# Performance work log

Hardware: AMD Instinct MI355X
Metric: run time of the kernel (lower is better)

The kernel has to match this reference:

```python
import jax, jax.numpy as jnp
import numpy as np

B, N = 2048, 4095  # batch, number of spherical points (cumsum length = N+1)


def setup_inputs() -> dict:
    key = jax.random.key(0)
    k1, k2, k3, k4, k5 = jax.random.split(key, 5)
    return {
        "origin_3D": jax.random.uniform(k1, (B, 3, 1), dtype=jnp.float32),
        "spherical_3D": jax.random.uniform(k2, (B, 3, N), dtype=jnp.float32),
        "origin_2D": jax.random.uniform(k3, (B, 3, 1), dtype=jnp.float32),
        "spherical_2D": jax.random.uniform(k4, (B, 3, N), dtype=jnp.float32),
        "deformation_field": jax.random.uniform(k5, (B, 2, N), dtype=jnp.float32),
    }


def _cart(origin, spherical):
    # spherical: [B, 3, N] with rows (r, theta, phi)
    r, theta, phi = spherical[:, 0, :], spherical[:, 1, :], spherical[:, 2, :]
    st = jnp.sin(theta)
    x = r * st * jnp.cos(phi)
    y = r * st * jnp.sin(phi)
    z = r * jnp.cos(theta)
    shape = jnp.stack((x, y, z), axis=1)            # [B, 3, N]
    full = jnp.concatenate((origin, shape), axis=2)  # [B, 3, N+1]
    # torch.matmul(full, triu(ones)) == prefix sum along the last axis
    return jnp.cumsum(full, axis=2)


def reference(origin_3D, spherical_3D, origin_2D, spherical_2D, deformation_field):
    spherical_3D_deformed = spherical_3D.at[:, 1:, :].add(deformation_field)
    original_cart = _cart(origin_2D, spherical_2D)            # [B, 3, N+1]
    deformed_cart = _cart(origin_3D, spherical_3D_deformed)   # [B, 3, N+1]
    per_pt = jnp.sum(jnp.abs(deformed_cart - original_cart), axis=1)  # [B, N+1]
    return jnp.sum(jnp.mean(per_pt, axis=1))  # scalar
```

## Files before the change

### kernel.cpp

```cpp
#include <hip/hip_runtime.h>


#define BATCH 2048
#define NPTS  4095
#define POS   4096
#define T     512
#define NW    8
#define M     8

__launch_bounds__(T, 2)
__global__ void mpd_loss_kernel(const float* __restrict__ origin3,
                                const float* __restrict__ sph3,
                                const float* __restrict__ origin2,
                                const float* __restrict__ sph2,
                                const float* __restrict__ def,
                                float* __restrict__ bsum) {
    __shared__ float ldsT[3][M][NW];
    __shared__ float wsum[NW];

    const int b    = blockIdx.x;
    const int t    = threadIdx.x;
    const int lane = t & 63;
    const int w    = t >> 6;

    const float* r3  = sph3 + (size_t)b * 3 * NPTS;
    const float* th3 = r3 + NPTS;
    const float* ph3 = th3 + NPTS;
    const float* r2  = sph2 + (size_t)b * 3 * NPTS;
    const float* th2 = r2 + NPTS;
    const float* ph2 = th2 + NPTS;
    const float* d0  = def + (size_t)b * 2 * NPTS;
    const float* d1  = d0 + NPTS;

    float vx[M], vy[M], vz[M];

    #pragma unroll
    for (int m = 0; m < M; ++m) {
        const int j = m * T + t;
        float dx, dy, dz;
        if (m == 0 && t == 0) {
            const float* o3 = origin3 + (size_t)b * 3;
            const float* o2 = origin2 + (size_t)b * 3;
            dx = o3[0] - o2[0];
            dy = o3[1] - o2[1];
            dz = o3[2] - o2[2];
        } else {
            const int n = j - 1;
            const float R3  = r3[n];
            const float Th3 = th3[n] + d0[n];
            const float Ph3 = ph3[n] + d1[n];
            const float R2  = r2[n];
            const float Th2 = th2[n];
            const float Ph2 = ph2[n];
            float s3, c3, sp3, cp3, s2, c2, sp2, cp2;
            __sincosf(Th3, &s3, &c3);
            __sincosf(Ph3, &sp3, &cp3);
            __sincosf(Th2, &s2, &c2);
            __sincosf(Ph2, &sp2, &cp2);
            const float rs3 = R3 * s3;
            const float rs2 = R2 * s2;
            dx = rs3 * cp3 - rs2 * cp2;
            dy = rs3 * sp3 - rs2 * sp2;
            dz = R3 * c3 - R2 * c2;
        }
        vx[m] = dx; vy[m] = dy; vz[m] = dz;
    }

    #pragma unroll
    for (int m = 0; m < M; ++m) {
        float x = vx[m], y = vy[m], z = vz[m];
        #pragma unroll
        for (int off = 1; off < 64; off <<= 1) {
            const float ux = __shfl_up(x, off, 64);
            const float uy = __shfl_up(y, off, 64);
            const float uz = __shfl_up(z, off, 64);
            if (lane >= off) { x += ux; y += uy; z += uz; }
        }
        vx[m] = x; vy[m] = y; vz[m] = z;
        if (lane == 63) {
            ldsT[0][m][w] = x;
            ldsT[1][m][w] = y;
            ldsT[2][m][w] = z;
        }
    }
    __syncthreads();

    float acc = 0.f;
    float rbx = 0.f, rby = 0.f, rbz = 0.f;
    #pragma unroll
    for (int m = 0; m < M; ++m) {
        float wx = 0.f, wy = 0.f, wz = 0.f;
        float tx = 0.f, ty = 0.f, tz = 0.f;
        #pragma unroll
        for (int ww = 0; ww < NW; ++ww) {
            const float a = ldsT[0][m][ww];
            const float c = ldsT[1][m][ww];
            const float e = ldsT[2][m][ww];
            if (ww < w) { wx += a; wy += c; wz += e; }
            tx += a; ty += c; tz += e;
        }
        acc += fabsf(rbx + wx + vx[m]) + fabsf(rby + wy + vy[m]) + fabsf(rbz + wz + vz[m]);
        rbx += tx; rby += ty; rbz += tz;
    }

    #pragma unroll
    for (int off = 32; off > 0; off >>= 1) acc += __shfl_down(acc, off, 64);
    if (lane == 0) wsum[w] = acc;
    __syncthreads();
    if (t == 0) {
        float s = 0.f;
        #pragma unroll
        for (int i = 0; i < NW; ++i) s += wsum[i];
        bsum[b] = s * (1.0f / POS);
    }
}

__launch_bounds__(256)
__global__ void reduce_kernel(const float* __restrict__ bsum, float* __restrict__ out) {
    const int t = threadIdx.x;
    float acc = 0.f;
    #pragma unroll
    for (int i = 0; i < BATCH / 256; ++i) acc += bsum[t + i * 256];
    #pragma unroll
    for (int off = 32; off > 0; off >>= 1) acc += __shfl_down(acc, off, 64);
    __shared__ float wsum[4];
    if ((t & 63) == 0) wsum[t >> 6] = acc;
    __syncthreads();
    if (t == 0) out[0] = wsum[0] + wsum[1] + wsum[2] + wsum[3];
}

extern "C" void kernel_launch(void* const* d_in, const int* in_sizes, int n_in,
                              void* d_out, int out_size, void* d_ws, size_t ws_size,
                              hipStream_t stream) {
    const float* origin3 = (const float*)d_in[0];
    const float* sph3    = (const float*)d_in[1];
    const float* origin2 = (const float*)d_in[2];
    const float* sph2    = (const float*)d_in[3];
    const float* def     = (const float*)d_in[4];
    float* out  = (float*)d_out;
    float* bsum = (float*)d_ws;

    mpd_loss_kernel<<<BATCH, T, 0, stream>>>(origin3, sph3, origin2, sph2, def, bsum);
    reduce_kernel<<<1, 256, 0, stream>>>(bsum, out);
}
```

Baseline: 272.0 us.

## Restructure prefix sum as per-thread serial chunks through padded LDS transpose

Each thread still computes its Cartesian deltas with coalesced global loads, but now writes them to padded LDS buffers. It then reads back a contiguous chunk of 8 elements, sums them serially, and runs only one wave-level shuffle scan on the chunk totals instead of eight. Each element's prefix is then rebuilt by serial accumulation. This cuts shuffle and scan instruction count roughly eightfold. In exchange it adds about 52KB of LDS per block and an extra barrier, and the occupancy hint is raised to 6 blocks, which the LDS footprint may not allow.

```diff
diff --git a/kernel.cpp b/kernel.cpp
--- a/kernel.cpp
+++ b/kernel.cpp
@@ -7,15 +7,20 @@
 #define T     512
 #define NW    8
 #define M     8
+#define CH    8
+#define BUFSZ 4352
 
-__launch_bounds__(T, 2)
+__launch_bounds__(T, 6)
 __global__ void mpd_loss_kernel(const float* __restrict__ origin3,
                                 const float* __restrict__ sph3,
                                 const float* __restrict__ origin2,
                                 const float* __restrict__ sph2,
                                 const float* __restrict__ def,
                                 float* __restrict__ bsum) {
-    __shared__ float ldsT[3][M][NW];
+    __shared__ float bufx[BUFSZ];
+    __shared__ float bufy[BUFSZ];
+    __shared__ float bufz[BUFSZ];
+    __shared__ float wtotx[NW], wtoty[NW], wtotz[NW];
     __shared__ float wsum[NW];
 
     const int b    = blockIdx.x;
@@ -31,8 +36,6 @@
     const float* ph2 = th2 + NPTS;
     const float* d0  = def + (size_t)b * 2 * NPTS;
     const float* d1  = d0 + NPTS;
-
-    float vx[M], vy[M], vz[M];
 
     #pragma unroll
     for (int m = 0; m < M; ++m) {
@@ -63,44 +66,49 @@
             dy = rs3 * sp3 - rs2 * sp2;
             dz = R3 * c3 - R2 * c2;
         }
-        vx[m] = dx; vy[m] = dy; vz[m] = dz;
-    }
-
-    #pragma unroll
-    for (int m = 0; m < M; ++m) {
-        float x = vx[m], y = vy[m], z = vz[m];
-        #pragma unroll
-        for (int off = 1; off < 64; off <<= 1) {
-            const float ux = __shfl_up(x, off, 64);
-            const float uy = __shfl_up(y, off, 64);
-            const float uz = __shfl_up(z, off, 64);
-            if (lane >= off) { x += ux; y += uy; z += uz; }
-        }
-        vx[m] = x; vy[m] = y; vz[m] = z;
-        if (lane == 63) {
-            ldsT[0][m][w] = x;
-            ldsT[1][m][w] = y;
-            ldsT[2][m][w] = z;
-        }
+        const int a = j + (j >> 4);
+        bufx[a] = dx;
+        bufy[a] = dy;
+        bufz[a] = dz;
     }
     __syncthreads();
 
+    const int jb = t * CH;
+    const int ba = jb + (jb >> 4);
+    float vx[CH], vy[CH], vz[CH];
+    float tx = 0.f, ty = 0.f, tz = 0.f;
+    #pragma unroll
+    for (int k = 0; k < CH; ++k) {
+        vx[k] = bufx[ba + k]; tx += vx[k];
+        vy[k] = bufy[ba + k]; ty += vy[k];
+        vz[k] = bufz[ba + k]; tz += vz[k];
+    }
+
+    float ix = tx, iy = ty, iz = tz;
+    #pragma unroll
+    for (int off = 1; off < 64; off <<= 1) {
+        const float ux = __shfl_up(ix, off, 64);
+        const float uy = __shfl_up(iy, off, 64);
+        const float uz = __shfl_up(iz, off, 64);
+        if (lane >= off) { ix += ux; iy += uy; iz += uz; }
+    }
+    if (lane == 63) { wtotx[w] = ix; wtoty[w] = iy; wtotz[w] = iz; }
+    __syncthreads();
+
+    float wox = 0.f, woy = 0.f, woz = 0.f;
+    #pragma unroll
+    for (int ww = 0; ww < NW; ++ww) {
+        if (ww < w) { wox += wtotx[ww]; woy += wtoty[ww]; woz += wtotz[ww]; }
+    }
+
+    float px = wox + (ix - tx);
+    float py = woy + (iy - ty);
+    float pz = woz + (iz - tz);
     float acc = 0.f;
-    float rbx = 0.f, rby = 0.f, rbz = 0.f;
     #pragma unroll
-    for (int m = 0; m < M; ++m) {
-        float wx = 0.f, wy = 0.f, wz = 0.f;
-        float tx = 0.f, ty = 0.f, tz = 0.f;
-        #pragma unroll
-        for (int ww = 0; ww < NW; ++ww) {
-            const float a = ldsT[0][m][ww];
-            const float c = ldsT[1][m][ww];
-            const float e = ldsT[2][m][ww];
-            if (ww < w) { wx += a; wy += c; wz += e; }
-            tx += a; ty += c; tz += e;
-        }
-        acc += fabsf(rbx + wx + vx[m]) + fabsf(rby + wy + vy[m]) + fabsf(rbz + wz + vz[m]);
-        rbx += tx; rby += ty; rbz += tz;
+    for (int k = 0; k < CH; ++k) {
+        px += vx[k]; py += vy[k]; pz += vz[k];
+        acc += fabsf(px) + fabsf(py) + fabsf(pz);
     }
 
     #pragma unroll
@@ -123,10 +131,10 @@
     for (int i = 0; i < BATCH / 256; ++i) acc += bsum[t + i * 256];
     #pragma unroll
     for (int off = 32; off > 0; off >>= 1) acc += __shfl_down(acc, off, 64);
-    __shared__ float wsum[4];
-    if ((t & 63) == 0) wsum[t >> 6] = acc;
+    __shared__ float wred[4];
+    if ((t & 63) == 0) wred[t >> 6] = acc;
     __syncthreads();
-    if (t == 0) out[0] = wsum[0] + wsum[1] + wsum[2] + wsum[3];
+    if (t == 0) out[0] = wred[0] + wred[1] + wred[2] + wred[3];
 }
 
 extern "C" void kernel_launch(void* const* d_in, const int* in_sizes, int n_in,
```

After: 267.7 us. About the same (-1.6%).
